# Optimization experiments

Measured on AMD Instinct MI355X. Metric: run time of the kernel, lower is better.

The kernel has to match this reference:

```python
import jax, jax.numpy as jnp
import numpy as np

N_NODES = 50000
N_EDGES = 1600000
D_FEAT = 64
N_SCALARS = 4
N_GRAPHS = 64
HIDDEN = 128
OUT = 128


def setup_inputs() -> dict:
    key = jax.random.key(0)
    ks = jax.random.split(key, 8)
    x = jax.random.normal(ks[0], (N_NODES, D_FEAT), dtype=jnp.float32)
    scalars = jax.random.normal(ks[1], (N_GRAPHS, N_SCALARS), dtype=jnp.float32)
    batch = jnp.sort(jax.random.randint(ks[2], (N_NODES,), 0, N_GRAPHS))
    edge_index = jax.random.randint(ks[3], (2, N_EDGES), 0, N_NODES)
    d_in = 2 * (D_FEAT + N_SCALARS)  # 136: EdgeConv-style cat([x_i, x_j - x_i])
    W1 = jax.random.normal(ks[4], (d_in, HIDDEN), dtype=jnp.float32) * (1.0 / np.sqrt(d_in))
    b1 = jnp.zeros((HIDDEN,), dtype=jnp.float32)
    W2 = jax.random.normal(ks[5], (HIDDEN, OUT), dtype=jnp.float32) * (1.0 / np.sqrt(HIDDEN))
    b2 = jnp.zeros((OUT,), dtype=jnp.float32)
    return {"x": x, "scalars": scalars, "batch": batch, "edge_index": edge_index,
            "W1": W1, "b1": b1, "W2": W2, "b2": b2}


def reference(x, scalars, batch, edge_index, W1, b1, W2, b2):
    # _reshape_scalars: gather per-graph scalars to nodes via batch index
    s = scalars[batch]                       # [N, n_scalars]
    h = jnp.concatenate([x, s], axis=-1)     # [N, d_feat + n_scalars]
    src, dst = edge_index[0], edge_index[1]  # edge j -> i (PyG convention)
    h_i = h[dst]                             # target node features [E, F]
    h_j = h[src]                             # source node features [E, F]
    m_in = jnp.concatenate([h_i, h_j - h_i], axis=-1)  # [E, 2F]
    m = jax.nn.relu(m_in @ W1 + b1) @ W2 + b2          # edge MLP [E, OUT]
    out = jax.ops.segment_sum(m, dst, num_segments=x.shape[0])  # add-aggregation
    return out
```

## Files before the change

kernel.cpp:

```cpp
#include <hip/hip_runtime.h>

#define N_NODES   50000
#define N_EDGES   1600000
#define D_FEAT    64
#define N_SCALARS 4
#define HIDDEN    128
#define OUT_DIM   128
#define UV_DIM    256

#define SLICE_SH  6
#define SLICE_N   (1 << SLICE_SH)
#define NSLICE    ((N_NODES + SLICE_N - 1) >> SLICE_SH)
#define CAP       2560
#define CAPQ      1024
#define CHUNK     4096

#define N_WAVES   (N_NODES / 16)
#define G1_BLOCKS ((N_WAVES + 3) / 4)
#define BIN_BLOCKS ((N_EDGES + CHUNK - 1) / CHUNK)

typedef __attribute__((ext_vector_type(8))) _Float16 half8;
typedef __attribute__((ext_vector_type(2))) _Float16 half2v;
typedef __attribute__((ext_vector_type(4))) float    f32x4;

__device__ __forceinline__ float wf_elem(const float* W1, int k, int j) {
    float wb = W1[(k + 68) * HIDDEN + (j & 127)];
    return (j < HIDDEN) ? (W1[k * HIDDEN + j] - wb) : wb;
}

__global__ __launch_bounds__(256) void prep_kernel(
    const float* __restrict__ W1, const float* __restrict__ b1,
    const float* __restrict__ W2, const float* __restrict__ scalars,
    _Float16* __restrict__ WfT, _Float16* __restrict__ W2T,
    float* __restrict__ SG, int* __restrict__ tails)
{
    const int idx = blockIdx.x * 256 + threadIdx.x;
    {   int j = idx >> 6, k = idx & 63;
        WfT[idx] = (_Float16)wf_elem(W1, k, j); }
    {   int j = idx >> 7, k = idx & 127;
        W2T[idx] = (_Float16)W2[k * OUT_DIM + j]; }
    {   int g = idx >> 8, j = idx & 255;
        float s = (j < HIDDEN) ? b1[j] : 0.f;
        #pragma unroll
        for (int t = 0; t < N_SCALARS; ++t)
            s = fmaf(scalars[g * N_SCALARS + t], wf_elem(W1, D_FEAT + t, j), s);
        SG[idx] = s; }
    if (idx < NSLICE) tails[idx] = 0;
}

__global__ __launch_bounds__(256) void gemm1_bin(
    const float* __restrict__ x, const int* __restrict__ batch,
    const _Float16* __restrict__ WfT, const float* __restrict__ SG,
    _Float16* __restrict__ Uh, _Float16* __restrict__ Vh,
    const int* __restrict__ ei, int* __restrict__ tails,
    unsigned* __restrict__ glist)
{
    __shared__ unsigned buf[CHUNK];
    __shared__ int hist[NSLICE];
    __shared__ int binStart[NSLICE];
    __shared__ int cursor[NSLICE];
    __shared__ int gbase[NSLICE];
    __shared__ int scanTmp[256];

    const int tid = threadIdx.x;

    if (blockIdx.x < G1_BLOCKS) {
        const int wid = (blockIdx.x * 256 + tid) >> 6;
        if (wid >= N_WAVES) return;
        const int lane = tid & 63;
        const int quad = lane >> 4;
        const int l15  = lane & 15;
        const int row0 = wid * 16;

        f32x4 acc[16];
        #pragma unroll
        for (int c = 0; c < 16; ++c) { f32x4 z = {0.f,0.f,0.f,0.f}; acc[c] = z; }

        const float* xrow = x + (row0 + l15) * D_FEAT;
        #pragma unroll
        for (int t = 0; t < 2; ++t) {
            const int k0 = 32 * t + quad * 8;
            float4 a0 = *(const float4*)(xrow + k0);
            float4 a1 = *(const float4*)(xrow + k0 + 4);
            half8 af;
            af[0] = (_Float16)a0.x; af[1] = (_Float16)a0.y;
            af[2] = (_Float16)a0.z; af[3] = (_Float16)a0.w;
            af[4] = (_Float16)a1.x; af[5] = (_Float16)a1.y;
            af[6] = (_Float16)a1.z; af[7] = (_Float16)a1.w;
            #pragma unroll
            for (int c = 0; c < 16; ++c) {
                half8 bf = *(const half8*)(WfT + (c * 16 + l15) * 64 + k0);
                acc[c] = __builtin_amdgcn_mfma_f32_16x16x32_f16(af, bf, acc[c], 0, 0, 0);
            }
        }

        int bg[4];
        #pragma unroll
        for (int j = 0; j < 4; ++j) bg[j] = batch[row0 + quad * 4 + j];

        #pragma unroll
        for (int c = 0; c < 16; ++c) {
            const int col = c * 16 + l15;
            #pragma unroll
            for (int j = 0; j < 4; ++j) {
                const int n = row0 + quad * 4 + j;
                float v = acc[c][j] + SG[bg[j] * UV_DIM + col];
                if (col < HIDDEN) Uh[(n << 7) + col] = (_Float16)v;
                else              Vh[(n << 7) + col - HIDDEN] = (_Float16)v;
            }
        }
        return;
    }

    const int e0  = (blockIdx.x - G1_BLOCKS) * CHUNK;
    const int nE  = min(CHUNK, N_EDGES - e0);

    for (int i = tid; i < NSLICE; i += 256) hist[i] = 0;
    __syncthreads();

    unsigned ent[CHUNK / 256];
    #pragma unroll
    for (int j = 0; j < CHUNK / 256; ++j) {
        int e = e0 + tid + j * 256;
        if (e < N_EDGES) {
            unsigned s = (unsigned)ei[e];
            unsigned d = (unsigned)ei[N_EDGES + e];
            ent[j] = (d << 16) | s;
            atomicAdd(&hist[d >> SLICE_SH], 1);
        } else {
            ent[j] = 0xFFFFFFFFu;
        }
    }
    __syncthreads();

    const int base4 = tid * 4;
    int loc[4];
    int sum = 0;
    #pragma unroll
    for (int k = 0; k < 4; ++k) {
        int b = base4 + k;
        loc[k] = (b < NSLICE) ? hist[b] : 0;
        sum += loc[k];
    }
    scanTmp[tid] = sum;
    __syncthreads();
    for (int d = 1; d < 256; d <<= 1) {
        int v = (tid >= d) ? scanTmp[tid - d] : 0;
        __syncthreads();
        scanTmp[tid] += v;
        __syncthreads();
    }
    int run = (tid == 0) ? 0 : scanTmp[tid - 1];
    #pragma unroll
    for (int k = 0; k < 4; ++k) {
        int b = base4 + k;
        if (b < NSLICE) { binStart[b] = run; cursor[b] = run; run += loc[k]; }
    }
    __syncthreads();

    #pragma unroll
    for (int j = 0; j < CHUNK / 256; ++j) {
        if (ent[j] != 0xFFFFFFFFu) {
            int sl = (int)(ent[j] >> (16 + SLICE_SH));
            int pos = atomicAdd(&cursor[sl], 1);
            buf[pos] = ent[j];
        }
    }
    __syncthreads();

    for (int s = tid; s < NSLICE; s += 256) {
        int c = hist[s];
        if (c > 0) gbase[s] = atomicAdd(&tails[s], c);
    }
    __syncthreads();

    for (int i = tid; i < nE; i += 256) {
        unsigned e = buf[i];
        int sl = (int)(e >> (16 + SLICE_SH));
        int di = gbase[sl] + (i - binStart[sl]);
        if (di < CAP) glist[(size_t)sl * CAP + di] = e;
    }
}

__global__ __launch_bounds__(256) void agg_gemm2(
    const unsigned* __restrict__ glist, const int* __restrict__ tails,
    const _Float16* __restrict__ Uh, const _Float16* __restrict__ Vh,
    const _Float16* __restrict__ W2T, const float* __restrict__ b2,
    float* __restrict__ out)
{
    __shared__ int h16[16];
    __shared__ int start16[16];
    __shared__ int cur16[16];
    __shared__ unsigned sbuf[CAPQ];
    __shared__ _Float16 aggA[16][136];

    const int slice = blockIdx.x;
    const int yq    = blockIdx.y;
    const int node0 = (slice << SLICE_SH) + yq * 16;
    const int tid   = threadIdx.x;
    const unsigned* lst = glist + (size_t)slice * CAP;
    const int cnt = min(tails[slice], CAP);

    if (tid < 16) h16[tid] = 0;
    __syncthreads();
    for (int i = tid; i < cnt; i += 256) {
        unsigned e = lst[i];
        int dl = (e >> 16) & 63;
        if ((dl >> 4) == yq) atomicAdd(&h16[dl & 15], 1);
    }
    __syncthreads();
    if (tid == 0) {
        int run = 0;
        #pragma unroll
        for (int b = 0; b < 16; ++b) {
            run = (run + 3) & ~3;
            start16[b] = run; cur16[b] = run;
            run += h16[b];
        }
    }
    __syncthreads();
    for (int i = tid; i < cnt; i += 256) {
        unsigned e = lst[i];
        int dl = (e >> 16) & 63;
        if ((dl >> 4) == yq) {
            int pos = atomicAdd(&cur16[dl & 15], 1);
            if (pos < CAPQ) sbuf[pos] = e & 0xFFFFu;
        }
    }
    __syncthreads();

    const int wave = tid >> 6;
    const int lane = tid & 63;
    const int quad = lane >> 4;
    const int l15  = lane & 15;
    const int c2   = lane * 2;
    const half2v zero = {(_Float16)0, (_Float16)0};

    #pragma unroll
    for (int i = 0; i < 4; ++i) {
        const int b = wave * 4 + i;
        const int n = node0 + b;
        half2v u2 = zero, acc2 = zero;
        int gb = start16[b];
        int gc = h16[b];
        if (n < N_NODES) u2 = *(const half2v*)(Uh + (n << 7) + c2);
        else gc = 0;
        int p = gb, pe = min(gb + gc, CAPQ);
        for (; p + 8 <= pe; p += 8) {
            uint4 q0 = *(const uint4*)&sbuf[p];
            uint4 q1 = *(const uint4*)&sbuf[p + 4];
            half2v v0 = *(const half2v*)(Vh + (q0.x << 7) + c2);
            half2v v1 = *(const half2v*)(Vh + (q0.y << 7) + c2);
            half2v v2 = *(const half2v*)(Vh + (q0.z << 7) + c2);
            half2v v3 = *(const half2v*)(Vh + (q0.w << 7) + c2);
            half2v v4 = *(const half2v*)(Vh + (q1.x << 7) + c2);
            half2v v5 = *(const half2v*)(Vh + (q1.y << 7) + c2);
            half2v v6 = *(const half2v*)(Vh + (q1.z << 7) + c2);
            half2v v7 = *(const half2v*)(Vh + (q1.w << 7) + c2);
            half2v m0 = __builtin_elementwise_max(u2 + v0, zero);
            half2v m1 = __builtin_elementwise_max(u2 + v1, zero);
            half2v m2 = __builtin_elementwise_max(u2 + v2, zero);
            half2v m3 = __builtin_elementwise_max(u2 + v3, zero);
            half2v m4 = __builtin_elementwise_max(u2 + v4, zero);
            half2v m5 = __builtin_elementwise_max(u2 + v5, zero);
            half2v m6 = __builtin_elementwise_max(u2 + v6, zero);
            half2v m7 = __builtin_elementwise_max(u2 + v7, zero);
            acc2 += ((m0 + m1) + (m2 + m3)) + ((m4 + m5) + (m6 + m7));
        }
        for (; p + 4 <= pe; p += 4) {
            uint4 q0 = *(const uint4*)&sbuf[p];
            half2v v0 = *(const half2v*)(Vh + (q0.x << 7) + c2);
            half2v v1 = *(const half2v*)(Vh + (q0.y << 7) + c2);
            half2v v2 = *(const half2v*)(Vh + (q0.z << 7) + c2);
            half2v v3 = *(const half2v*)(Vh + (q0.w << 7) + c2);
            acc2 += (__builtin_elementwise_max(u2 + v0, zero)
                   + __builtin_elementwise_max(u2 + v1, zero))
                  + (__builtin_elementwise_max(u2 + v2, zero)
                   + __builtin_elementwise_max(u2 + v3, zero));
        }
        for (; p < pe; ++p) {
            int s0 = (int)sbuf[p];
            half2v v0 = *(const half2v*)(Vh + (s0 << 7) + c2);
            acc2 += __builtin_elementwise_max(u2 + v0, zero);
        }
        *(half2v*)&aggA[b][c2] = acc2;
    }
    __syncthreads();

    f32x4 accm[2];
    {   f32x4 z = {0.f,0.f,0.f,0.f}; accm[0] = z; accm[1] = z; }
    #pragma unroll
    for (int t = 0; t < 4; ++t) {
        const int k0 = 32 * t + quad * 8;
        half8 af = *(const half8*)&aggA[l15][k0];
        #pragma unroll
        for (int c = 0; c < 2; ++c) {
            const int ct = wave * 2 + c;
            half8 bf = *(const half8*)(W2T + ((ct * 16 + l15) << 7) + k0);
            accm[c] = __builtin_amdgcn_mfma_f32_16x16x32_f16(af, bf, accm[c], 0, 0, 0);
        }
    }
    int dgj[4];
    #pragma unroll
    for (int j = 0; j < 4; ++j) dgj[j] = h16[quad * 4 + j];

    #pragma unroll
    for (int c = 0; c < 2; ++c) {
        const int col = (wave * 2 + c) * 16 + l15;
        const float bb = b2[col];
        #pragma unroll
        for (int j = 0; j < 4; ++j) {
            const int n = node0 + quad * 4 + j;
            if (n < N_NODES)
                out[(size_t)n * OUT_DIM + col] = accm[c][j] + bb * (float)dgj[j];
        }
    }
}

extern "C" void kernel_launch(void* const* d_in, const int* in_sizes, int n_in,
                              void* d_out, int out_size, void* d_ws, size_t ws_size,
                              hipStream_t stream)
{
    const float* x       = (const float*)d_in[0];
    const float* scalars = (const float*)d_in[1];
    const int*   batch   = (const int*)d_in[2];
    const int*   ei      = (const int*)d_in[3];
    const float* W1      = (const float*)d_in[4];
    const float* b1      = (const float*)d_in[5];
    const float* W2      = (const float*)d_in[6];
    const float* b2      = (const float*)d_in[7];
    float*       out     = (float*)d_out;

    _Float16* Uh    = (_Float16*)d_ws;
    _Float16* Vh    = Uh + (size_t)N_NODES * HIDDEN;
    unsigned* glist = (unsigned*)(Vh + (size_t)N_NODES * HIDDEN);
    _Float16* WfT   = (_Float16*)(glist + (size_t)NSLICE * CAP);
    _Float16* W2T   = WfT + 256 * 64;
    float*    SG    = (float*)(W2T + 128 * 128);
    int*      tails = (int*)(SG + 64 * UV_DIM);

    prep_kernel<<<64, 256, 0, stream>>>(W1, b1, W2, scalars, WfT, W2T, SG, tails);

    gemm1_bin<<<G1_BLOCKS + BIN_BLOCKS, 256, 0, stream>>>(
        x, batch, WfT, SG, Uh, Vh, ei, tails, glist);

    agg_gemm2<<<dim3(NSLICE, 4), 256, 0, stream>>>(
        glist, tails, Uh, Vh, W2T, b2, out);
}
```

Baseline: 196.9 us.

## Process each wave's four nodes as one merged edge stream with node tags

Edges are packed contiguously in shared memory with the local node index stored in the upper bits, so each wave walks the combined edge list of its four nodes in one loop and switches accumulators when the node tag changes. U rows are staged into shared memory up front, and aggA is zero-initialised so nodes with no edges still read as zero. The aim is to remove per-node tail loops and padding and to keep more gathers in flight (16 per iteration). In exchange, every edge now carries a data-dependent branch and a compare, which adds scalar work in the inner loop.

Measured after the change: 204.3 us. +3.8%, slower.

```diff
diff --git a/kernel.cpp b/kernel.cpp
--- a/kernel.cpp
+++ b/kernel.cpp
@@ -192,6 +192,7 @@
     __shared__ int start16[16];
     __shared__ int cur16[16];
     __shared__ unsigned sbuf[CAPQ];
+    __shared__ _Float16 uL[16][128];
     __shared__ _Float16 aggA[16][136];
 
     const int slice = blockIdx.x;
@@ -213,18 +214,35 @@
         int run = 0;
         #pragma unroll
         for (int b = 0; b < 16; ++b) {
-            run = (run + 3) & ~3;
             start16[b] = run; cur16[b] = run;
             run += h16[b];
         }
     }
     __syncthreads();
+
     for (int i = tid; i < cnt; i += 256) {
         unsigned e = lst[i];
         int dl = (e >> 16) & 63;
         if ((dl >> 4) == yq) {
             int pos = atomicAdd(&cur16[dl & 15], 1);
-            if (pos < CAPQ) sbuf[pos] = e & 0xFFFFu;
+            if (pos < CAPQ) sbuf[pos] = (e & 0xFFFFu) | ((unsigned)(dl & 15) << 16);
+        }
+    }
+    {
+        int t = tid;
+        for (int rep = 0; rep < 4; ++rep, t += 256) {
+            int r = t >> 6, c = t & 63;
+            int n = node0 + r;
+            unsigned w = 0;
+            if (n < N_NODES) w = ((const unsigned*)(Uh + (n << 7)))[c];
+            ((unsigned*)&uL[r][0])[(r * 64 + c) - r * 64] = 0;
+            *(unsigned*)&uL[r][c * 2] = w;
+        }
+    }
+    {
+        for (int t = tid; t < 16 * 64; t += 256) {
+            int r = t >> 6, c = t & 63;
+            *(unsigned*)&aggA[r][c * 2] = 0;
         }
     }
     __syncthreads();
@@ -235,55 +253,57 @@
     const int l15  = lane & 15;
     const int c2   = lane * 2;
     const half2v zero = {(_Float16)0, (_Float16)0};
-
-    #pragma unroll
-    for (int i = 0; i < 4; ++i) {
-        const int b = wave * 4 + i;
-        const int n = node0 + b;
-        half2v u2 = zero, acc2 = zero;
-        int gb = start16[b];
-        int gc = h16[b];
-        if (n < N_NODES) u2 = *(const half2v*)(Uh + (n << 7) + c2);
-        else gc = 0;
-        int p = gb, pe = min(gb + gc, CAPQ);
-        for (; p + 8 <= pe; p += 8) {
+    const _Float16* Vc = Vh + c2;
+
+    {
+        const int b0 = wave * 4;
+        int rb = start16[b0];
+        int re = min(start16[b0 + 3] + h16[b0 + 3], CAPQ);
+        int cur = -1;
+        half2v u2 = zero, acc = zero;
+
+        auto load1 = [&](unsigned e) -> half2v {
+            return *(const half2v*)(Vc + ((e & 0xFFFFu) << 7));
+        };
+        auto proc = [&](unsigned e, half2v v) {
+            int dl = (int)(e >> 16);
+            if (dl != cur) {
+                if (cur >= 0) *(half2v*)&aggA[cur][c2] = acc;
+                cur = dl; acc = zero;
+                u2 = *(const half2v*)&uL[dl][c2];
+            }
+            acc += __builtin_elementwise_max(u2 + v, zero);
+        };
+
+        int p = rb;
+        while (p < re && (p & 3)) {
+            unsigned e = sbuf[p++];
+            proc(e, load1(e));
+        }
+        for (; p + 16 <= re; p += 16) {
             uint4 q0 = *(const uint4*)&sbuf[p];
             uint4 q1 = *(const uint4*)&sbuf[p + 4];
-            half2v v0 = *(const half2v*)(Vh + (q0.x << 7) + c2);
-            half2v v1 = *(const half2v*)(Vh + (q0.y << 7) + c2);
-            half2v v2 = *(const half2v*)(Vh + (q0.z << 7) + c2);
-            half2v v3 = *(const half2v*)(Vh + (q0.w << 7) + c2);
-            half2v v4 = *(const half2v*)(Vh + (q1.x << 7) + c2);
-            half2v v5 = *(const half2v*)(Vh + (q1.y << 7) + c2);
-            half2v v6 = *(const half2v*)(Vh + (q1.z << 7) + c2);
-            half2v v7 = *(const half2v*)(Vh + (q1.w << 7) + c2);
-            half2v m0 = __builtin_elementwise_max(u2 + v0, zero);
-            half2v m1 = __builtin_elementwise_max(u2 + v1, zero);
-            half2v m2 = __builtin_elementwise_max(u2 + v2, zero);
-            half2v m3 = __builtin_elementwise_max(u2 + v3, zero);
-            half2v m4 = __builtin_elementwise_max(u2 + v4, zero);
-            half2v m5 = __builtin_elementwise_max(u2 + v5, zero);
-            half2v m6 = __builtin_elementwise_max(u2 + v6, zero);
-            half2v m7 = __builtin_elementwise_max(u2 + v7, zero);
-            acc2 += ((m0 + m1) + (m2 + m3)) + ((m4 + m5) + (m6 + m7));
-        }
-        for (; p + 4 <= pe; p += 4) {
+            uint4 q2 = *(const uint4*)&sbuf[p + 8];
+            uint4 q3 = *(const uint4*)&sbuf[p + 12];
+            half2v v0  = load1(q0.x), v1  = load1(q0.y), v2  = load1(q0.z), v3  = load1(q0.w);
+            half2v v4  = load1(q1.x), v5  = load1(q1.y), v6  = load1(q1.z), v7  = load1(q1.w);
+            half2v v8  = load1(q2.x), v9  = load1(q2.y), v10 = load1(q2.z), v11 = load1(q2.w);
+            half2v v12 = load1(q3.x), v13 = load1(q3.y), v14 = load1(q3.z), v15 = load1(q3.w);
+            proc(q0.x, v0);  proc(q0.y, v1);  proc(q0.z, v2);  proc(q0.w, v3);
+            proc(q1.x, v4);  proc(q1.y, v5);  proc(q1.z, v6);  proc(q1.w, v7);
+            proc(q2.x, v8);  proc(q2.y, v9);  proc(q2.z, v10); proc(q2.w, v11);
+            proc(q3.x, v12); proc(q3.y, v13); proc(q3.z, v14); proc(q3.w, v15);
+        }
+        for (; p + 4 <= re; p += 4) {
             uint4 q0 = *(const uint4*)&sbuf[p];
-            half2v v0 = *(const half2v*)(Vh + (q0.x << 7) + c2);
-            half2v v1 = *(const half2v*)(Vh + (q0.y << 7) + c2);
-            half2v v2 = *(const half2v*)(Vh + (q0.z << 7) + c2);
-            half2v v3 = *(const half2v*)(Vh + (q0.w << 7) + c2);
-            acc2 += (__builtin_elementwise_max(u2 + v0, zero)
-                   + __builtin_elementwise_max(u2 + v1, zero))
-                  + (__builtin_elementwise_max(u2 + v2, zero)
-                   + __builtin_elementwise_max(u2 + v3, zero));
-        }
-        for (; p < pe; ++p) {
-            int s0 = (int)sbuf[p];
-            half2v v0 = *(const half2v*)(Vh + (s0 << 7) + c2);
-            acc2 += __builtin_elementwise_max(u2 + v0, zero);
-        }
-        *(half2v*)&aggA[b][c2] = acc2;
+            half2v v0 = load1(q0.x), v1 = load1(q0.y), v2 = load1(q0.z), v3 = load1(q0.w);
+            proc(q0.x, v0); proc(q0.y, v1); proc(q0.z, v2); proc(q0.w, v3);
+        }
+        for (; p < re; ++p) {
+            unsigned e = sbuf[p];
+            proc(e, load1(e));
+        }
+        if (cur >= 0) *(half2v*)&aggA[cur][c2] = acc;
     }
     __syncthreads();
 
```
